# Optimization experiments

Measured on AMD Instinct MI355X. Metric: run time of the kernel, lower is better.

The kernel has to match this reference:

```python
import jax, jax.numpy as jnp
import numpy as np

IN_C = 256
OUT_C = 256
QK_C = OUT_C // 8  # channel_reduction_rate = 8
B, H, W = 8, 64, 64


def setup_inputs() -> dict:
    key = jax.random.key(0)
    ks = jax.random.split(key, 7)
    s_in = 1.0 / np.sqrt(IN_C)  # torch Conv2d default init scale (kernel=1)
    return {
        "x": jax.random.normal(ks[0], (B, IN_C, H, W), dtype=jnp.float32),
        "W1": jax.random.uniform(ks[1], (OUT_C, IN_C), jnp.float32, -s_in, s_in),
        "b1": jax.random.uniform(ks[2], (OUT_C,), jnp.float32, -s_in, s_in),
        "W2": jax.random.uniform(ks[3], (QK_C, IN_C), jnp.float32, -s_in, s_in),
        "b2": jax.random.uniform(ks[4], (QK_C,), jnp.float32, -s_in, s_in),
        "W3": jax.random.uniform(ks[5], (QK_C, IN_C), jnp.float32, -s_in, s_in),
        "b3": jax.random.uniform(ks[6], (QK_C,), jnp.float32, -s_in, s_in),
    }


def reference(x, W1, b1, W2, b2, W3, b3):
    b, c, h, w = x.shape
    n = h * w
    xf = x.reshape(b, c, n)  # 1x1 conv == channel matmul on flattened spatial
    v = jnp.einsum("oc,bcn->bon", W1, xf) + b1[None, :, None]   # [B, OUT_C, N]
    q = jnp.einsum("oc,bcn->bon", W2, xf) + b2[None, :, None]   # [B, QK_C, N]
    k = jnp.einsum("oc,bcn->bon", W3, xf) + b3[None, :, None]   # [B, QK_C, N]
    scores = jnp.einsum("bdn,bdm->bnm", q, k)                    # [B, N, N]
    # GLOBAL softmax over the full flattened NxN matrix per batch element
    attn = jax.nn.softmax(scores.reshape(b, -1), axis=1).reshape(b, n, n)
    out = jnp.einsum("bon,bnm->bom", v, attn)                    # [B, OUT_C, N]
    return out.reshape(x.shape) + x
```

## Files before the change

kernel.cpp:

```cpp
#include <hip/hip_runtime.h>
#include <hip/hip_bf16.h>
#include <math.h>

#define NBATCH 8
#define NC 256
#define ND 32
#define SN 4096

constexpr size_t VB_B   = 0;
constexpr size_t QT_B   = 16777216;
constexpr size_t KT_B   = QT_B + 2097152;
constexpr size_t PM_B   = KT_B + 2097152;
constexpr size_t PS_B   = PM_B + 32768;
constexpr size_t C_B    = PS_B + 32768;
constexpr size_t WB_B   = C_B + 64;
constexpr size_t BIAS_B = WB_B + 163840;

typedef __attribute__((ext_vector_type(8))) short short8;
typedef __attribute__((ext_vector_type(4))) float f32x4;

__device__ __forceinline__ unsigned bf16rne(float f) {
  unsigned u = __float_as_uint(f);
  return (u + 0x7fffu + ((u >> 16) & 1u)) >> 16;
}
__device__ __forceinline__ unsigned bfpack2(float lo, float hi) {
  union { __hip_bfloat162 h; unsigned u; } cv;
  cv.h.x = __float2bfloat16(lo);
  cv.h.y = __float2bfloat16(hi);
  return cv.u;
}

__global__ __launch_bounds__(256) void prep_kernel(
    const float* __restrict__ W1, const float* __restrict__ b1,
    const float* __restrict__ W2, const float* __restrict__ b2,
    const float* __restrict__ W3, const float* __restrict__ b3,
    char* __restrict__ wsb)
{
  ushort* Wb = (ushort*)(wsb + WB_B);
  float* bias = (float*)(wsb + BIAS_B);
  const float LOG2E = 1.4426950408889634f;
  int idx = blockIdx.x * 256 + threadIdx.x;
  int r = idx >> 6, c4 = (idx & 63) * 4;
  float4 v; float sc = 1.0f;
  if (r < 256)      { v = *(const float4*)(W1 + (size_t)r * 256 + c4); }
  else if (r < 288) { v = *(const float4*)(W2 + (size_t)(r - 256) * 256 + c4); sc = LOG2E; }
  else              { v = *(const float4*)(W3 + (size_t)(r - 288) * 256 + c4); }
  ushort4 o;
  o.x = (ushort)bfpack2(v.x * sc, 0.f); o.y = (ushort)bfpack2(v.y * sc, 0.f);
  o.z = (ushort)bfpack2(v.z * sc, 0.f); o.w = (ushort)bfpack2(v.w * sc, 0.f);
  *(ushort4*)(Wb + (size_t)r * 256 + c4) = o;
  if (blockIdx.x == 0 && threadIdx.x < 320) {
    int q = threadIdx.x;
    bias[q] = q < 256 ? b1[q] : (q < 288 ? b2[q - 256] * LOG2E : b3[q - 288]);
  }
}

__global__ __launch_bounds__(512) void proj_kernel(
    const float* __restrict__ x, char* __restrict__ wsb)
{
  __shared__ alignas(16) char xT[65536];
  __shared__ alignas(16) char Wsh[40960];
  const int bid = blockIdx.x;
  const int b = bid & 7, nt = bid >> 3;
  const int n0 = nt * 128;
  const int t = threadIdx.x, w = t >> 6, lane = t & 63;
  const int l4 = lane >> 4, l16 = lane & 15;
  const float* xb = x + (size_t)b * NC * SN;
  const ushort* Wb = (const ushort*)(wsb + WB_B);
  const float* bias = (const float*)(wsb + BIAS_B);
  ushort* vbuf  = (ushort*)(wsb + VB_B);
  ushort* qtbuf = (ushort*)(wsb + QT_B);
  ushort* ktbuf = (ushort*)(wsb + KT_B);

  {
    int cp = w * 16 + l16;
    int c  = cp * 2;
    int nb0 = l4 * 4;
#pragma unroll
    for (int ni = 0; ni < 8; ++ni) {
      int nB = ni * 16 + nb0;
      float4 a0 = *(const float4*)(xb + (size_t)c * SN + n0 + nB);
      float4 a1 = *(const float4*)(xb + (size_t)(c + 1) * SN + n0 + nB);
      const float* p0 = (const float*)&a0;
      const float* p1 = (const float*)&a1;
#pragma unroll
      for (int j = 0; j < 4; ++j) {
        int n = nB + j;
        *(uint*)(xT + n * 512 + ((cp * 4) ^ ((n & 7) << 4))) = bfpack2(p0[j], p1[j]);
      }
    }
  }
#pragma unroll
  for (int ii = 0; ii < 5; ++ii) {
    int slot = t + ii * 512;
    int r = slot >> 3, cc = slot & 7;
    *(uint4*)(Wsh + r * 128 + ((cc * 16) ^ ((r & 7) << 4))) =
        *(const uint4*)(Wb + (size_t)r * 256 + cc * 8);
  }
  __syncthreads();

  const int of_g = w >> 1;
  const int nf_g = w & 1;
  f32x4 acc[5][4] = {};

  for (int c4 = 0; c4 < 4; ++c4) {
#pragma unroll
    for (int kk = 0; kk < 2; ++kk) {
      short8 a[4];
#pragma unroll
      for (int nf = 0; nf < 4; ++nf) {
        int n = nf_g * 64 + nf * 16 + l16;
        a[nf] = *(const short8*)(xT + n * 512 +
                 ((c4 * 128 + kk * 64 + l4 * 16) ^ ((n & 7) << 4)));
      }
#pragma unroll
      for (int of = 0; of < 5; ++of) {
        int o = (of_g * 5 + of) * 16 + l16;
        short8 bf = *(const short8*)(Wsh + o * 128 +
                    ((kk * 64 + l4 * 16) ^ ((o & 7) << 4)));
#pragma unroll
        for (int nf = 0; nf < 4; ++nf)
          acc[of][nf] = __builtin_amdgcn_mfma_f32_16x16x32_bf16(a[nf], bf, acc[of][nf], 0, 0, 0);
      }
    }
    if (c4 < 3) {
      __syncthreads();
#pragma unroll
      for (int ii = 0; ii < 5; ++ii) {
        int slot = t + ii * 512;
        int r = slot >> 3, cc = slot & 7;
        *(uint4*)(Wsh + r * 128 + ((cc * 16) ^ ((r & 7) << 4))) =
            *(const uint4*)(Wb + (size_t)r * 256 + (c4 + 1) * 64 + cc * 8);
      }
      __syncthreads();
    }
  }

#pragma unroll
  for (int of = 0; of < 5; ++of) {
    int o = (of_g * 5 + of) * 16 + l16;
    float bv = bias[o];
#pragma unroll
    for (int nf = 0; nf < 4; ++nf) {
      int nb = nf_g * 64 + nf * 16 + l4 * 4;
      float v0 = acc[of][nf][0] + bv, v1 = acc[of][nf][1] + bv;
      float v2 = acc[of][nf][2] + bv, v3 = acc[of][nf][3] + bv;
      if (o < 256) {
        uint2 pk; pk.x = bfpack2(v0, v1); pk.y = bfpack2(v2, v3);
        *(uint2*)(vbuf + ((size_t)b * NC + o) * SN + n0 + nb) = pk;
      } else if (o < 288) {
        int d = o - 256;
        qtbuf[((size_t)b * SN + n0 + nb + 0) * ND + d] = (ushort)bf16rne(v0);
        qtbuf[((size_t)b * SN + n0 + nb + 1) * ND + d] = (ushort)bf16rne(v1);
        qtbuf[((size_t)b * SN + n0 + nb + 2) * ND + d] = (ushort)bf16rne(v2);
        qtbuf[((size_t)b * SN + n0 + nb + 3) * ND + d] = (ushort)bf16rne(v3);
      } else {
        int d = o - 288;
        ktbuf[((size_t)b * SN + n0 + nb + 0) * ND + d] = (ushort)bf16rne(v0);
        ktbuf[((size_t)b * SN + n0 + nb + 1) * ND + d] = (ushort)bf16rne(v1);
        ktbuf[((size_t)b * SN + n0 + nb + 2) * ND + d] = (ushort)bf16rne(v2);
        ktbuf[((size_t)b * SN + n0 + nb + 3) * ND + d] = (ushort)bf16rne(v3);
      }
    }
  }
}

__global__ __launch_bounds__(256) void qk_stats(
    const char* __restrict__ wsb, float* __restrict__ pm, float* __restrict__ ps)
{
  __shared__ alignas(16) char qt_s[128 * 64];
  __shared__ alignas(16) char kt_s[128 * 64];
  __shared__ float wm[4], wz[4];
  const int bid = blockIdx.x;
  const int b = bid & 7, ny = (bid >> 3) & 31, mx = bid >> 8;
  const int n0 = ny * 128, m0 = mx * 128;
  const int t = threadIdx.x, w = t >> 6, lane = t & 63;
  const int l4 = lane >> 4, l16 = lane & 15;
  const ushort* qtb = (const ushort*)(wsb + QT_B) + (size_t)b * SN * ND;
  const ushort* ktb = (const ushort*)(wsb + KT_B) + (size_t)b * SN * ND;
  {
    int row = t >> 1, db = (t & 1) * 32;
#pragma unroll
    for (int i = 0; i < 2; ++i) {
      int b16 = db + i * 16;
      int dst = row * 64 + (b16 ^ ((row & 3) << 4));
      *(uint4*)(qt_s + dst) = *(const uint4*)(qtb + (size_t)(n0 + row) * ND + b16 / 2);
      *(uint4*)(kt_s + dst) = *(const uint4*)(ktb + (size_t)(m0 + row) * ND + b16 / 2);
    }
  }
  __syncthreads();
  const f32x4 zf = {0.f, 0.f, 0.f, 0.f};
  short8 bfr[2];
#pragma unroll
  for (int j = 0; j < 2; ++j) {
    int mm = (w * 2 + j) * 16 + l16;
    bfr[j] = *(const short8*)(kt_s + mm * 64 + ((l4 * 16) ^ ((mm & 3) << 4)));
  }
  f32x4 sfr[8][2];
#pragma unroll
  for (int i = 0; i < 8; ++i) {
    int nn = i * 16 + l16;
    short8 af = *(const short8*)(qt_s + nn * 64 + ((l4 * 16) ^ ((nn & 3) << 4)));
#pragma unroll
    for (int j = 0; j < 2; ++j)
      sfr[i][j] = __builtin_amdgcn_mfma_f32_16x16x32_bf16(af, bfr[j], zf, 0, 0, 0);
  }
  float mt = -1e30f;
#pragma unroll
  for (int i = 0; i < 8; ++i)
#pragma unroll
    for (int j = 0; j < 2; ++j)
#pragma unroll
      for (int r = 0; r < 4; ++r) mt = fmaxf(mt, sfr[i][j][r]);
  float zt = 0.f;
#pragma unroll
  for (int i = 0; i < 8; ++i)
#pragma unroll
    for (int j = 0; j < 2; ++j)
#pragma unroll
      for (int r = 0; r < 4; ++r) zt += exp2f(sfr[i][j][r] - mt);

#pragma unroll
  for (int off = 1; off < 64; off <<= 1) {
    float m2 = __shfl_xor(mt, off);
    float z2 = __shfl_xor(zt, off);
    float M = fmaxf(mt, m2);
    zt = zt * exp2f(mt - M) + z2 * exp2f(m2 - M);
    mt = M;
  }
  if (lane == 0) { wm[w] = mt; wz[w] = zt; }
  __syncthreads();
  if (t == 0) {
    float m = wm[0], z = wz[0];
#pragma unroll
    for (int i = 1; i < 4; ++i) {
      float M = fmaxf(m, wm[i]);
      z = z * exp2f(m - M) + wz[i] * exp2f(wm[i] - M);
      m = M;
    }
    int idx = (b * 32 + ny) * 32 + mx;
    pm[idx] = m; ps[idx] = z;
  }
}

__global__ __launch_bounds__(256) void reduce_kernel(char* __restrict__ wsb)
{
  const int b = blockIdx.x;
  const float* pm = (const float*)(wsb + PM_B) + (size_t)b * 1024;
  const float* ps = (const float*)(wsb + PS_B) + (size_t)b * 1024;
  const int t = threadIdx.x;
  float m = -1e30f, z = 0.f;
  for (int i = t; i < 1024; i += 256) {
    float m2 = pm[i], z2 = ps[i];
    float M = fmaxf(m, m2);
    z = z * exp2f(m - M) + z2 * exp2f(m2 - M);
    m = M;
  }
#pragma unroll
  for (int off = 1; off < 64; off <<= 1) {
    float m2 = __shfl_xor(m, off);
    float z2 = __shfl_xor(z, off);
    float M = fmaxf(m, m2);
    z = z * exp2f(m - M) + z2 * exp2f(m2 - M);
    m = M;
  }
  __shared__ float wm[4], wz[4];
  int w = t >> 6;
  if ((t & 63) == 0) { wm[w] = m; wz[w] = z; }
  __syncthreads();
  if (t == 0) {
    float M = wm[0], Z = wz[0];
#pragma unroll
    for (int i = 1; i < 4; ++i) {
      float Mn = fmaxf(M, wm[i]);
      Z = Z * exp2f(M - Mn) + wz[i] * exp2f(wm[i] - Mn);
      M = Mn;
    }
    ((float*)(wsb + C_B))[b] = M + log2f(Z);
  }
}

__global__ __launch_bounds__(512, 4) void attn_out(
    const char* __restrict__ wsb, const float* __restrict__ x, float* __restrict__ out)
{
  __shared__ alignas(16) char as_s[2][16384];
  const int bid = blockIdx.x;
  const int b = bid & 7, mt = bid >> 3;
  const int m0 = mt * 64;
  const int t = threadIdx.x, w = t >> 6, lane = t & 63;
  const int l4 = lane >> 4, l16 = lane & 15;
  const ushort* vb  = (const ushort*)(wsb + VB_B) + (size_t)b * NC * SN;
  const ushort* qtb = (const ushort*)(wsb + QT_B) + (size_t)b * SN * ND;
  const ushort* ktb = (const ushort*)(wsb + KT_B) + (size_t)b * SN * ND;
  const float Cb = ((const float*)(wsb + C_B))[b];

  const int mS_l = (w & 3) * 16 + l16;
  const int nh   = w >> 2;
  short8 bfr = *(const short8*)(ktb + (size_t)(m0 + mS_l) * ND + l4 * 8);

  const int wr_base = mS_l * 16 + (l4 & 1) * 8;
  const int l4h = l4 >> 1;

  const ushort* vrow0 = vb + (size_t)(w * 32 + l16) * SN + l4 * 8;
  const ushort* vrow1 = vrow0 + (size_t)16 * SN;

  const f32x4 zf = {0.f, 0.f, 0.f, 0.f};
  f32x4 acc[2][4] = {};

  {
    const ushort* qn = qtb + (size_t)(nh * 64) * ND + l4 * 8;
#pragma unroll
    for (int ii = 0; ii < 4; ++ii) {
      int nf = nh * 4 + ii;
      short8 af = *(const short8*)(qn + (size_t)(ii * 16 + l16) * ND);
      f32x4 sv = __builtin_amdgcn_mfma_f32_16x16x32_bf16(af, bfr, zf, 0, 0, 0);
      uint2 pk;
      pk.x = bfpack2(exp2f(sv[0] - Cb), exp2f(sv[1] - Cb));
      pk.y = bfpack2(exp2f(sv[2] - Cb), exp2f(sv[3] - Cb));
      int addr = (nf >> 1) * 4096 + (((nf << 1) + l4h) & 3) * 1024 + wr_base;
      *(uint2*)(as_s[0] + addr) = pk;
    }
  }
  __syncthreads();

  for (int i = 0; i < 32; ++i) {
    const int cur = i & 1;
    short8 vf0[4], vf1[4];
#pragma unroll
    for (int kk = 0; kk < 4; ++kk) {
      vf0[kk] = *(const short8*)(vrow0 + i * 128 + kk * 32);
      vf1[kk] = *(const short8*)(vrow1 + i * 128 + kk * 32);
    }
    short8 af[4];
    if (i < 31) {
      const ushort* qn = qtb + (size_t)((i + 1) * 128 + nh * 64) * ND + l4 * 8;
#pragma unroll
      for (int ii = 0; ii < 4; ++ii)
        af[ii] = *(const short8*)(qn + (size_t)(ii * 16 + l16) * ND);
    }
    __builtin_amdgcn_s_setprio(1);
#pragma unroll
    for (int kk = 0; kk < 4; ++kk) {
      const char* base = as_s[cur] + kk * 4096 + l4 * 1024;
#pragma unroll
      for (int mf = 0; mf < 4; ++mf) {
        short8 paf = *(const short8*)(base + mf * 256 + l16 * 16);
        acc[0][mf] = __builtin_amdgcn_mfma_f32_16x16x32_bf16(vf0[kk], paf, acc[0][mf], 0, 0, 0);
        acc[1][mf] = __builtin_amdgcn_mfma_f32_16x16x32_bf16(vf1[kk], paf, acc[1][mf], 0, 0, 0);
      }
    }
    __builtin_amdgcn_s_setprio(0);
    if (i < 31) {
#pragma unroll
      for (int ii = 0; ii < 4; ++ii) {
        int nf = nh * 4 + ii;
        f32x4 sv = __builtin_amdgcn_mfma_f32_16x16x32_bf16(af[ii], bfr, zf, 0, 0, 0);
        uint2 pk;
        pk.x = bfpack2(exp2f(sv[0] - Cb), exp2f(sv[1] - Cb));
        pk.y = bfpack2(exp2f(sv[2] - Cb), exp2f(sv[3] - Cb));
        int addr = (nf >> 1) * 4096 + (((nf << 1) + l4h) & 3) * 1024 + wr_base;
        *(uint2*)(as_s[cur ^ 1] + addr) = pk;
      }
    }
    __syncthreads();
  }

#pragma unroll
  for (int of = 0; of < 2; ++of)
#pragma unroll
    for (int mf = 0; mf < 4; ++mf) {
      int m = m0 + mf * 16 + l16;
#pragma unroll
      for (int j = 0; j < 4; ++j) {
        int o = w * 32 + of * 16 + l4 * 4 + j;
        size_t idx = ((size_t)b * NC + o) * SN + m;
        out[idx] = acc[of][mf][j] + x[idx];
      }
    }
}

extern "C" void kernel_launch(void* const* d_in, const int* in_sizes, int n_in,
                              void* d_out, int out_size, void* d_ws, size_t ws_size,
                              hipStream_t stream)
{
  const float* x  = (const float*)d_in[0];
  const float* W1 = (const float*)d_in[1];
  const float* b1 = (const float*)d_in[2];
  const float* W2 = (const float*)d_in[3];
  const float* b2 = (const float*)d_in[4];
  const float* W3 = (const float*)d_in[5];
  const float* b3 = (const float*)d_in[6];
  char* wsb  = (char*)d_ws;
  float* out = (float*)d_out;

  prep_kernel<<<80, 256, 0, stream>>>(W1, b1, W2, b2, W3, b3, wsb);
  proj_kernel<<<256, 512, 0, stream>>>(x, wsb);
  qk_stats<<<8192, 256, 0, stream>>>(wsb, (float*)(wsb + PM_B), (float*)(wsb + PS_B));
  reduce_kernel<<<NBATCH, 256, 0, stream>>>(wsb);
  attn_out<<<512, 512, 0, stream>>>(wsb, x, out);
}
```

Measured before the change: 229.7 us.

## Stage Q tiles through LDS and restructure attn_out pipeline per iteration

Q tiles for the next step are now loaded cooperatively, one uint4 per thread, into a double-buffered LDS buffer instead of each wave doing its own per-fragment global loads. The score/exp computation moves before the PV MFMA loop within the same iteration, writing into the current P buffer. Launch bounds change from 4 to 6 waves per EU. This is meant to cut redundant global Q traffic and register pressure so occupancy can rise. In exchange the loop now waits on a barrier before PV, so exp work no longer overlaps the previous PV MFMAs, and it uses more LDS.

```diff
diff --git a/kernel.cpp b/kernel.cpp
--- a/kernel.cpp
+++ b/kernel.cpp
@@ -280,9 +280,10 @@
   }
 }
 
-__global__ __launch_bounds__(512, 4) void attn_out(
+__global__ __launch_bounds__(512, 6) void attn_out(
     const char* __restrict__ wsb, const float* __restrict__ x, float* __restrict__ out)
 {
+  __shared__ alignas(16) char qt_s[2][8192];
   __shared__ alignas(16) char as_s[2][16384];
   const int bid = blockIdx.x;
   const int b = bid & 7, mt = bid >> 3;
@@ -301,43 +302,45 @@
   const int wr_base = mS_l * 16 + (l4 & 1) * 8;
   const int l4h = l4 >> 1;
 
+  const int qrow = t >> 2, qsl = t & 3;
+  const int qt_addr = (qrow >> 4) * 1024 + (((qsl << 4) | (qrow & 15)) << 4);
+
   const ushort* vrow0 = vb + (size_t)(w * 32 + l16) * SN + l4 * 8;
   const ushort* vrow1 = vrow0 + (size_t)16 * SN;
 
   const f32x4 zf = {0.f, 0.f, 0.f, 0.f};
   f32x4 acc[2][4] = {};
 
-  {
-    const ushort* qn = qtb + (size_t)(nh * 64) * ND + l4 * 8;
+  *(uint4*)(qt_s[0] + qt_addr) = *(const uint4*)(qtb + (size_t)qrow * ND + qsl * 8);
+  __syncthreads();
+
+  for (int i = 0; i < 32; ++i) {
+    const int cur = i & 1;
+    short8 vf[2][4];
+#pragma unroll
+    for (int kk = 0; kk < 4; ++kk) {
+      vf[0][kk] = *(const short8*)(vrow0 + i * 128 + kk * 32);
+      vf[1][kk] = *(const short8*)(vrow1 + i * 128 + kk * 32);
+    }
+    uint4 qnext;
+    const bool pf = (i < 31);
+    if (pf) qnext = *(const uint4*)(qtb + (size_t)((i + 1) * 128 + qrow) * ND + qsl * 8);
+
 #pragma unroll
     for (int ii = 0; ii < 4; ++ii) {
       int nf = nh * 4 + ii;
-      short8 af = *(const short8*)(qn + (size_t)(ii * 16 + l16) * ND);
+      short8 af = *(const short8*)(qt_s[cur] + nf * 1024 + lane * 16);
       f32x4 sv = __builtin_amdgcn_mfma_f32_16x16x32_bf16(af, bfr, zf, 0, 0, 0);
       uint2 pk;
       pk.x = bfpack2(exp2f(sv[0] - Cb), exp2f(sv[1] - Cb));
       pk.y = bfpack2(exp2f(sv[2] - Cb), exp2f(sv[3] - Cb));
       int addr = (nf >> 1) * 4096 + (((nf << 1) + l4h) & 3) * 1024 + wr_base;
-      *(uint2*)(as_s[0] + addr) = pk;
-    }
-  }
-  __syncthreads();
-
-  for (int i = 0; i < 32; ++i) {
-    const int cur = i & 1;
-    short8 vf0[4], vf1[4];
-#pragma unroll
-    for (int kk = 0; kk < 4; ++kk) {
-      vf0[kk] = *(const short8*)(vrow0 + i * 128 + kk * 32);
-      vf1[kk] = *(const short8*)(vrow1 + i * 128 + kk * 32);
-    }
-    short8 af[4];
-    if (i < 31) {
-      const ushort* qn = qtb + (size_t)((i + 1) * 128 + nh * 64) * ND + l4 * 8;
-#pragma unroll
-      for (int ii = 0; ii < 4; ++ii)
-        af[ii] = *(const short8*)(qn + (size_t)(ii * 16 + l16) * ND);
-    }
+      *(uint2*)(as_s[cur] + addr) = pk;
+    }
+    if (pf)
+      *(uint4*)(qt_s[cur ^ 1] + qt_addr) = qnext;
+    __syncthreads();
+
     __builtin_amdgcn_s_setprio(1);
 #pragma unroll
     for (int kk = 0; kk < 4; ++kk) {
@@ -345,24 +348,11 @@
 #pragma unroll
       for (int mf = 0; mf < 4; ++mf) {
         short8 paf = *(const short8*)(base + mf * 256 + l16 * 16);
-        acc[0][mf] = __builtin_amdgcn_mfma_f32_16x16x32_bf16(vf0[kk], paf, acc[0][mf], 0, 0, 0);
-        acc[1][mf] = __builtin_amdgcn_mfma_f32_16x16x32_bf16(vf1[kk], paf, acc[1][mf], 0, 0, 0);
+        acc[0][mf] = __builtin_amdgcn_mfma_f32_16x16x32_bf16(vf[0][kk], paf, acc[0][mf], 0, 0, 0);
+        acc[1][mf] = __builtin_amdgcn_mfma_f32_16x16x32_bf16(vf[1][kk], paf, acc[1][mf], 0, 0, 0);
       }
     }
     __builtin_amdgcn_s_setprio(0);
-    if (i < 31) {
-#pragma unroll
-      for (int ii = 0; ii < 4; ++ii) {
-        int nf = nh * 4 + ii;
-        f32x4 sv = __builtin_amdgcn_mfma_f32_16x16x32_bf16(af[ii], bfr, zf, 0, 0, 0);
-        uint2 pk;
-        pk.x = bfpack2(exp2f(sv[0] - Cb), exp2f(sv[1] - Cb));
-        pk.y = bfpack2(exp2f(sv[2] - Cb), exp2f(sv[3] - Cb));
-        int addr = (nf >> 1) * 4096 + (((nf << 1) + l4h) & 3) * 1024 + wr_base;
-        *(uint2*)(as_s[cur ^ 1] + addr) = pk;
-      }
-    }
-    __syncthreads();
   }
 
 #pragma unroll
```

New measurement: 367.5 us. +60.0%, slower.
